# Kernel tuning notes

Measured on AMD Instinct MI355X. Metric: run time of the kernel, lower is better.

## Reference

```python
import jax, jax.numpy as jnp
import numpy as np

BATCH, SEQLEN, DMODEL, DSTATE = 8, 2048, 1024, 16


def setup_inputs() -> dict:
    key = jax.random.key(0)
    ks = jax.random.split(key, 6)
    u = jax.random.normal(ks[0], (BATCH, SEQLEN, DMODEL), dtype=jnp.float32)
    # delta (discretization step) is positive in Mamba (post-softplus); sample small positive values
    delta = jax.random.uniform(ks[1], (BATCH, SEQLEN, DMODEL), dtype=jnp.float32, minval=0.001, maxval=0.1)
    # A must be negative so exp(delta*A) is a decay in (0,1)
    A = -jnp.exp(jax.random.normal(ks[2], (DMODEL, DSTATE), dtype=jnp.float32) * 0.5)
    B_mat = jax.random.normal(ks[3], (BATCH, SEQLEN, DSTATE), dtype=jnp.float32)
    C_mat = jax.random.normal(ks[4], (BATCH, SEQLEN, DSTATE), dtype=jnp.float32)
    D_vec = jax.random.normal(ks[5], (DMODEL,), dtype=jnp.float32)
    return {"u": u, "delta": delta, "A": A, "B_mat": B_mat, "C_mat": C_mat, "D_vec": D_vec}


def reference(u, delta, A, B_mat, C_mat, D_vec):
    """Selective scan (Mamba-style):
       h_t = exp(delta_t * A) * h_{t-1} + (delta_t * u_t) * B_t
       y_t = <h_t, C_t> + D * u_t
    u, delta: [B, L, D]; A: [D, N]; B_mat, C_mat: [B, L, N]; D_vec: [D].
    """
    def scan_fn(h, xs):
        u_t, d_t, b_t, c_t = xs                      # [B,D],[B,D],[B,N],[B,N]
        dA = jnp.exp(d_t[..., None] * A)             # [B,D,N] decay
        dBu = (d_t * u_t)[..., None] * b_t[:, None, :]  # [B,D,N] driven input
        h = dA * h + dBu                             # [B,D,N]
        y = jnp.einsum('bdn,bn->bd', h, c_t)         # [B,D]
        return h, y

    h0 = jnp.zeros((u.shape[0], u.shape[2], A.shape[1]), dtype=u.dtype)
    # time-leading layout for lax.scan
    xs = (jnp.swapaxes(u, 0, 1), jnp.swapaxes(delta, 0, 1),
          jnp.swapaxes(B_mat, 0, 1), jnp.swapaxes(C_mat, 0, 1))
    _, ys = jax.lax.scan(scan_fn, h0, xs)            # ys: [L,B,D]
    y = jnp.swapaxes(ys, 0, 1) + u * D_vec           # [B,L,D]
    return y
```

## Files before the change

### kernel.cpp

```cpp
#include <hip/hip_runtime.h>

#define BATCH   8
#define SEQLEN  2048
#define DMODEL  1024
#define DSTATE  16
#define NCHUNK  16
#define TCHUNK  (SEQLEN / NCHUNK)
#define BLOCK   256
#define LOG2E   1.4426950408889634f

__global__ __launch_bounds__(BLOCK) void ssm_phaseA(
    const float* __restrict__ u,  const float* __restrict__ de,
    const float* __restrict__ A,  const float* __restrict__ Bm,
    float* __restrict__ ws_h, float* __restrict__ ws_d)
{
    __shared__ float sB[TCHUNK * DSTATE];
    const int tid = threadIdx.x;
    const int d   = blockIdx.x * BLOCK + tid;
    const int c   = blockIdx.y;
    const int b   = blockIdx.z;
    const int t0  = c * TCHUNK;

    {
        const float4* src = (const float4*)(Bm + (size_t)(b * SEQLEN + t0) * DSTATE);
        float4* dst = (float4*)sB;
        #pragma unroll
        for (int i = 0; i < (TCHUNK * DSTATE / 4) / BLOCK; ++i)
            dst[tid + i * BLOCK] = src[tid + i * BLOCK];
    }
    __syncthreads();

    float A2[DSTATE];
    #pragma unroll
    for (int n = 0; n < DSTATE; n += 4) {
        float4 a4 = *(const float4*)(A + (size_t)d * DSTATE + n);
        A2[n+0] = a4.x * LOG2E; A2[n+1] = a4.y * LOG2E;
        A2[n+2] = a4.z * LOG2E; A2[n+3] = a4.w * LOG2E;
    }
    float h[DSTATE];
    #pragma unroll
    for (int n = 0; n < DSTATE; ++n) h[n] = 0.f;
    float dsum = 0.f;

    const float* up = u  + (size_t)(b * SEQLEN + t0) * DMODEL + d;
    const float* dp = de + (size_t)(b * SEQLEN + t0) * DMODEL + d;

    for (int t = 0; t < TCHUNK; ++t) {
        float dl = dp[(size_t)t * DMODEL];
        float uu = up[(size_t)t * DMODEL];
        dsum += dl;
        float du = dl * uu;
        #pragma unroll
        for (int n = 0; n < DSTATE; n += 4) {
            float4 b4 = *(const float4*)(sB + t * DSTATE + n);
            h[n+0] = __builtin_amdgcn_exp2f(dl * A2[n+0]) * h[n+0] + du * b4.x;
            h[n+1] = __builtin_amdgcn_exp2f(dl * A2[n+1]) * h[n+1] + du * b4.y;
            h[n+2] = __builtin_amdgcn_exp2f(dl * A2[n+2]) * h[n+2] + du * b4.z;
            h[n+3] = __builtin_amdgcn_exp2f(dl * A2[n+3]) * h[n+3] + du * b4.w;
        }
    }

    float* wh = ws_h + (size_t)(b * NCHUNK + c) * DSTATE * DMODEL + d;
    #pragma unroll
    for (int n = 0; n < DSTATE; ++n) wh[(size_t)n * DMODEL] = h[n];
    ws_d[(size_t)(b * NCHUNK + c) * DMODEL + d] = dsum;
}

__global__ __launch_bounds__(BLOCK) void ssm_phaseC(
    const float* __restrict__ u,  const float* __restrict__ de,
    const float* __restrict__ A,  const float* __restrict__ Bm,
    const float* __restrict__ Cm, const float* __restrict__ Dv,
    const float* __restrict__ ws_h, const float* __restrict__ ws_d,
    float* __restrict__ y)
{
    __shared__ float sB[TCHUNK * DSTATE];
    __shared__ float sC[TCHUNK * DSTATE];
    const int tid = threadIdx.x;
    const int d   = blockIdx.x * BLOCK + tid;
    const int c   = blockIdx.y;
    const int b   = blockIdx.z;
    const int t0  = c * TCHUNK;

    {
        const float4* srcB = (const float4*)(Bm + (size_t)(b * SEQLEN + t0) * DSTATE);
        const float4* srcC = (const float4*)(Cm + (size_t)(b * SEQLEN + t0) * DSTATE);
        float4* dstB = (float4*)sB;
        float4* dstC = (float4*)sC;
        #pragma unroll
        for (int i = 0; i < (TCHUNK * DSTATE / 4) / BLOCK; ++i) {
            dstB[tid + i * BLOCK] = srcB[tid + i * BLOCK];
            dstC[tid + i * BLOCK] = srcC[tid + i * BLOCK];
        }
    }
    __syncthreads();

    float A2[DSTATE];
    #pragma unroll
    for (int n = 0; n < DSTATE; n += 4) {
        float4 a4 = *(const float4*)(A + (size_t)d * DSTATE + n);
        A2[n+0] = a4.x * LOG2E; A2[n+1] = a4.y * LOG2E;
        A2[n+2] = a4.z * LOG2E; A2[n+3] = a4.w * LOG2E;
    }

    float h[DSTATE];
    #pragma unroll
    for (int n = 0; n < DSTATE; ++n) h[n] = 0.f;
    for (int j = 0; j < c; ++j) {
        float dsj = ws_d[(size_t)(b * NCHUNK + j) * DMODEL + d];
        const float* wh = ws_h + (size_t)(b * NCHUNK + j) * DSTATE * DMODEL + d;
        #pragma unroll
        for (int n = 0; n < DSTATE; ++n)
            h[n] = __builtin_amdgcn_exp2f(A2[n] * dsj) * h[n] + wh[(size_t)n * DMODEL];
    }

    const float Dd = Dv[d];
    const float* up = u  + (size_t)(b * SEQLEN + t0) * DMODEL + d;
    const float* dp = de + (size_t)(b * SEQLEN + t0) * DMODEL + d;
    float* yp = y + (size_t)(b * SEQLEN + t0) * DMODEL + d;

    for (int t = 0; t < TCHUNK; ++t) {
        float dl = dp[(size_t)t * DMODEL];
        float uu = up[(size_t)t * DMODEL];
        float du  = dl * uu;
        float acc = Dd * uu;
        #pragma unroll
        for (int n = 0; n < DSTATE; n += 4) {
            float4 b4 = *(const float4*)(sB + t * DSTATE + n);
            float4 c4 = *(const float4*)(sC + t * DSTATE + n);
            h[n+0] = __builtin_amdgcn_exp2f(dl * A2[n+0]) * h[n+0] + du * b4.x;
            h[n+1] = __builtin_amdgcn_exp2f(dl * A2[n+1]) * h[n+1] + du * b4.y;
            h[n+2] = __builtin_amdgcn_exp2f(dl * A2[n+2]) * h[n+2] + du * b4.z;
            h[n+3] = __builtin_amdgcn_exp2f(dl * A2[n+3]) * h[n+3] + du * b4.w;
            acc += h[n+0] * c4.x;
            acc += h[n+1] * c4.y;
            acc += h[n+2] * c4.z;
            acc += h[n+3] * c4.w;
        }
        yp[(size_t)t * DMODEL] = acc;
    }
}

__global__ __launch_bounds__(BLOCK) void ssm_naive(
    const float* __restrict__ u,  const float* __restrict__ de,
    const float* __restrict__ A,  const float* __restrict__ Bm,
    const float* __restrict__ Cm, const float* __restrict__ Dv,
    float* __restrict__ y)
{
    const int tid = threadIdx.x;
    const int d   = blockIdx.x * BLOCK + tid;
    const int b   = blockIdx.z;

    float A2[DSTATE];
    #pragma unroll
    for (int n = 0; n < DSTATE; n += 4) {
        float4 a4 = *(const float4*)(A + (size_t)d * DSTATE + n);
        A2[n+0] = a4.x * LOG2E; A2[n+1] = a4.y * LOG2E;
        A2[n+2] = a4.z * LOG2E; A2[n+3] = a4.w * LOG2E;
    }
    float h[DSTATE];
    #pragma unroll
    for (int n = 0; n < DSTATE; ++n) h[n] = 0.f;
    const float Dd = Dv[d];

    const float* up = u  + (size_t)b * SEQLEN * DMODEL + d;
    const float* dp = de + (size_t)b * SEQLEN * DMODEL + d;
    float* yp = y + (size_t)b * SEQLEN * DMODEL + d;

    for (int t = 0; t < SEQLEN; ++t) {
        float dl = dp[(size_t)t * DMODEL];
        float uu = up[(size_t)t * DMODEL];
        float du  = dl * uu;
        float acc = Dd * uu;
        const float* bp = Bm + (size_t)(b * SEQLEN + t) * DSTATE;
        const float* cp = Cm + (size_t)(b * SEQLEN + t) * DSTATE;
        #pragma unroll
        for (int n = 0; n < DSTATE; n += 4) {
            float4 b4 = *(const float4*)(bp + n);
            float4 c4 = *(const float4*)(cp + n);
            h[n+0] = __builtin_amdgcn_exp2f(dl * A2[n+0]) * h[n+0] + du * b4.x;
            h[n+1] = __builtin_amdgcn_exp2f(dl * A2[n+1]) * h[n+1] + du * b4.y;
            h[n+2] = __builtin_amdgcn_exp2f(dl * A2[n+2]) * h[n+2] + du * b4.z;
            h[n+3] = __builtin_amdgcn_exp2f(dl * A2[n+3]) * h[n+3] + du * b4.w;
            acc += h[n+0] * c4.x;
            acc += h[n+1] * c4.y;
            acc += h[n+2] * c4.z;
            acc += h[n+3] * c4.w;
        }
        yp[(size_t)t * DMODEL] = acc;
    }
}

extern "C" void kernel_launch(void* const* d_in, const int* in_sizes, int n_in,
                              void* d_out, int out_size, void* d_ws, size_t ws_size,
                              hipStream_t stream) {
    const float* u  = (const float*)d_in[0];
    const float* de = (const float*)d_in[1];
    const float* A  = (const float*)d_in[2];
    const float* Bm = (const float*)d_in[3];
    const float* Cm = (const float*)d_in[4];
    const float* Dv = (const float*)d_in[5];
    float* y = (float*)d_out;

    const size_t n_wsh = (size_t)BATCH * NCHUNK * DSTATE * DMODEL;
    const size_t n_wsd = (size_t)BATCH * NCHUNK * DMODEL;
    const size_t need  = (n_wsh + n_wsd) * sizeof(float);

    if (ws_size >= need) {
        float* ws_h = (float*)d_ws;
        float* ws_d = ws_h + n_wsh;
        dim3 grid(DMODEL / BLOCK, NCHUNK, BATCH);
        ssm_phaseA<<<grid, BLOCK, 0, stream>>>(u, de, A, Bm, ws_h, ws_d);
        ssm_phaseC<<<grid, BLOCK, 0, stream>>>(u, de, A, Bm, Cm, Dv, ws_h, ws_d, y);
    } else {
        dim3 grid(DMODEL / BLOCK, 1, BATCH);
        ssm_naive<<<grid, BLOCK, 0, stream>>>(u, de, A, Bm, Cm, Dv, y);
    }
}
```

Measured before the change: 140.3 us.

## Add inter-chunk prefix-scan kernel and raise chunk count to 64

Adds a middle kernel that does the sequential carry propagation across chunks once per (batch, state, channel) and writes each chunk's incoming state in place. Phase C then loads its initial state directly instead of redoing an O(c) recombination loop per chunk. With that redundant work gone, the chunk count rises from 16 to 64, giving four times as many blocks for parallelism. The cost is an extra kernel launch and a workspace four times larger, which needs a larger ws_size, with a fallback to 16 chunks.

```diff
diff --git a/kernel.cpp b/kernel.cpp
--- a/kernel.cpp
+++ b/kernel.cpp
@@ -4,29 +4,28 @@
 #define SEQLEN  2048
 #define DMODEL  1024
 #define DSTATE  16
-#define NCHUNK  16
-#define TCHUNK  (SEQLEN / NCHUNK)
 #define BLOCK   256
 #define LOG2E   1.4426950408889634f
 
+template<int NC>
 __global__ __launch_bounds__(BLOCK) void ssm_phaseA(
     const float* __restrict__ u,  const float* __restrict__ de,
     const float* __restrict__ A,  const float* __restrict__ Bm,
     float* __restrict__ ws_h, float* __restrict__ ws_d)
 {
-    __shared__ float sB[TCHUNK * DSTATE];
+    constexpr int TC = SEQLEN / NC;
+    __shared__ float sB[TC * DSTATE];
     const int tid = threadIdx.x;
     const int d   = blockIdx.x * BLOCK + tid;
     const int c   = blockIdx.y;
     const int b   = blockIdx.z;
-    const int t0  = c * TCHUNK;
+    const int t0  = c * TC;
 
     {
         const float4* src = (const float4*)(Bm + (size_t)(b * SEQLEN + t0) * DSTATE);
         float4* dst = (float4*)sB;
-        #pragma unroll
-        for (int i = 0; i < (TCHUNK * DSTATE / 4) / BLOCK; ++i)
-            dst[tid + i * BLOCK] = src[tid + i * BLOCK];
+        for (int i = tid; i < TC * DSTATE / 4; i += BLOCK)
+            dst[i] = src[i];
     }
     __syncthreads();
 
@@ -45,7 +44,8 @@
     const float* up = u  + (size_t)(b * SEQLEN + t0) * DMODEL + d;
     const float* dp = de + (size_t)(b * SEQLEN + t0) * DMODEL + d;
 
-    for (int t = 0; t < TCHUNK; ++t) {
+    #pragma unroll 2
+    for (int t = 0; t < TC; ++t) {
         float dl = dp[(size_t)t * DMODEL];
         float uu = up[(size_t)t * DMODEL];
         dsum += dl;
@@ -60,36 +60,63 @@
         }
     }
 
-    float* wh = ws_h + (size_t)(b * NCHUNK + c) * DSTATE * DMODEL + d;
+    float* wh = ws_h + (size_t)(b * NC + c) * DSTATE * DMODEL + d;
     #pragma unroll
     for (int n = 0; n < DSTATE; ++n) wh[(size_t)n * DMODEL] = h[n];
-    ws_d[(size_t)(b * NCHUNK + c) * DMODEL + d] = dsum;
-}
-
+    ws_d[(size_t)(b * NC + c) * DMODEL + d] = dsum;
+}
+
+template<int NC>
+__global__ __launch_bounds__(BLOCK) void ssm_phaseB(
+    const float* __restrict__ A,
+    float* __restrict__ ws_h, const float* __restrict__ ws_d)
+{
+    const int gid = blockIdx.x * BLOCK + threadIdx.x;
+    const int d  = gid % DMODEL;
+    const int bn = gid / DMODEL;
+    const int n  = bn % DSTATE;
+    const int b  = bn / DSTATE;
+
+    const float a2 = A[(size_t)d * DSTATE + n] * LOG2E;
+    float h = 0.f;
+    size_t ih = (size_t)b * NC * DSTATE * DMODEL + (size_t)n * DMODEL + d;
+    size_t id = (size_t)b * NC * DMODEL + d;
+
+    #pragma unroll 4
+    for (int c = 0; c < NC; ++c) {
+        float hl = ws_h[ih];
+        float ds = ws_d[id];
+        ws_h[ih] = h;
+        h = __builtin_amdgcn_exp2f(a2 * ds) * h + hl;
+        ih += (size_t)DSTATE * DMODEL;
+        id += DMODEL;
+    }
+}
+
+template<int NC>
 __global__ __launch_bounds__(BLOCK) void ssm_phaseC(
     const float* __restrict__ u,  const float* __restrict__ de,
     const float* __restrict__ A,  const float* __restrict__ Bm,
     const float* __restrict__ Cm, const float* __restrict__ Dv,
-    const float* __restrict__ ws_h, const float* __restrict__ ws_d,
-    float* __restrict__ y)
-{
-    __shared__ float sB[TCHUNK * DSTATE];
-    __shared__ float sC[TCHUNK * DSTATE];
+    const float* __restrict__ ws_h, float* __restrict__ y)
+{
+    constexpr int TC = SEQLEN / NC;
+    __shared__ float sB[TC * DSTATE];
+    __shared__ float sC[TC * DSTATE];
     const int tid = threadIdx.x;
     const int d   = blockIdx.x * BLOCK + tid;
     const int c   = blockIdx.y;
     const int b   = blockIdx.z;
-    const int t0  = c * TCHUNK;
+    const int t0  = c * TC;
 
     {
         const float4* srcB = (const float4*)(Bm + (size_t)(b * SEQLEN + t0) * DSTATE);
         const float4* srcC = (const float4*)(Cm + (size_t)(b * SEQLEN + t0) * DSTATE);
         float4* dstB = (float4*)sB;
         float4* dstC = (float4*)sC;
-        #pragma unroll
-        for (int i = 0; i < (TCHUNK * DSTATE / 4) / BLOCK; ++i) {
-            dstB[tid + i * BLOCK] = srcB[tid + i * BLOCK];
-            dstC[tid + i * BLOCK] = srcC[tid + i * BLOCK];
+        for (int i = tid; i < TC * DSTATE / 4; i += BLOCK) {
+            dstB[i] = srcB[i];
+            dstC[i] = srcC[i];
         }
     }
     __syncthreads();
@@ -103,14 +130,10 @@
     }
 
     float h[DSTATE];
-    #pragma unroll
-    for (int n = 0; n < DSTATE; ++n) h[n] = 0.f;
-    for (int j = 0; j < c; ++j) {
-        float dsj = ws_d[(size_t)(b * NCHUNK + j) * DMODEL + d];
-        const float* wh = ws_h + (size_t)(b * NCHUNK + j) * DSTATE * DMODEL + d;
-        #pragma unroll
-        for (int n = 0; n < DSTATE; ++n)
-            h[n] = __builtin_amdgcn_exp2f(A2[n] * dsj) * h[n] + wh[(size_t)n * DMODEL];
+    {
+        const float* wh = ws_h + (size_t)(b * NC + c) * DSTATE * DMODEL + d;
+        #pragma unroll
+        for (int n = 0; n < DSTATE; ++n) h[n] = wh[(size_t)n * DMODEL];
     }
 
     const float Dd = Dv[d];
@@ -118,7 +141,8 @@
     const float* dp = de + (size_t)(b * SEQLEN + t0) * DMODEL + d;
     float* yp = y + (size_t)(b * SEQLEN + t0) * DMODEL + d;
 
-    for (int t = 0; t < TCHUNK; ++t) {
+    #pragma unroll 2
+    for (int t = 0; t < TC; ++t) {
         float dl = dp[(size_t)t * DMODEL];
         float uu = up[(size_t)t * DMODEL];
         float du  = dl * uu;
@@ -190,6 +214,17 @@
     }
 }
 
+template<int NC>
+static void launch_chunked(const float* u, const float* de, const float* A,
+                           const float* Bm, const float* Cm, const float* Dv,
+                           float* ws_h, float* ws_d, float* y, hipStream_t stream) {
+    dim3 grid(DMODEL / BLOCK, NC, BATCH);
+    ssm_phaseA<NC><<<grid, BLOCK, 0, stream>>>(u, de, A, Bm, ws_h, ws_d);
+    dim3 gridB((BATCH * DSTATE * DMODEL) / BLOCK, 1, 1);
+    ssm_phaseB<NC><<<gridB, BLOCK, 0, stream>>>(A, ws_h, ws_d);
+    ssm_phaseC<NC><<<grid, BLOCK, 0, stream>>>(u, de, A, Bm, Cm, Dv, ws_h, y);
+}
+
 extern "C" void kernel_launch(void* const* d_in, const int* in_sizes, int n_in,
                               void* d_out, int out_size, void* d_ws, size_t ws_size,
                               hipStream_t stream) {
@@ -201,16 +236,19 @@
     const float* Dv = (const float*)d_in[5];
     float* y = (float*)d_out;
 
-    const size_t n_wsh = (size_t)BATCH * NCHUNK * DSTATE * DMODEL;
-    const size_t n_wsd = (size_t)BATCH * NCHUNK * DMODEL;
-    const size_t need  = (n_wsh + n_wsd) * sizeof(float);
-
-    if (ws_size >= need) {
+    auto need = [](int nc) {
+        return ((size_t)BATCH * nc * DSTATE * DMODEL +
+                (size_t)BATCH * nc * DMODEL) * sizeof(float);
+    };
+
+    if (ws_size >= need(64)) {
         float* ws_h = (float*)d_ws;
-        float* ws_d = ws_h + n_wsh;
-        dim3 grid(DMODEL / BLOCK, NCHUNK, BATCH);
-        ssm_phaseA<<<grid, BLOCK, 0, stream>>>(u, de, A, Bm, ws_h, ws_d);
-        ssm_phaseC<<<grid, BLOCK, 0, stream>>>(u, de, A, Bm, Cm, Dv, ws_h, ws_d, y);
+        float* ws_d = ws_h + (size_t)BATCH * 64 * DSTATE * DMODEL;
+        launch_chunked<64>(u, de, A, Bm, Cm, Dv, ws_h, ws_d, y, stream);
+    } else if (ws_size >= need(16)) {
+        float* ws_h = (float*)d_ws;
+        float* ws_d = ws_h + (size_t)BATCH * 16 * DSTATE * DMODEL;
+        launch_chunked<16>(u, de, A, Bm, Cm, Dv, ws_h, ws_d, y, stream);
     } else {
         dim3 grid(DMODEL / BLOCK, 1, BATCH);
         ssm_naive<<<grid, BLOCK, 0, stream>>>(u, de, A, Bm, Cm, Dv, y);
```

Measured after the change: 116.4 us. 17.1% less time.
